# Performance work log

Hardware: AMD Instinct MI355X
Metric: run time of the kernel (lower is better)

Reference implementation:

```python
import jax, jax.numpy as jnp
import numpy as np

B, T, C, H, W = 4, 8, 128, 96, 96
D = 64  # d_model

def setup_inputs() -> dict:
    key = jax.random.key(0)
    ks = jax.random.split(key, 7)
    return {
        "x": jax.random.normal(ks[0], (B, T, C, H, W), dtype=jnp.float32),
        "Wq": jax.random.normal(ks[1], (D, C), dtype=jnp.float32) * (1.0 / np.sqrt(C)),
        "bq": jax.random.normal(ks[2], (D,), dtype=jnp.float32) * 0.01,
        "Wk": jax.random.normal(ks[3], (D, C), dtype=jnp.float32) * (1.0 / np.sqrt(C)),
        "bk": jax.random.normal(ks[4], (D,), dtype=jnp.float32) * 0.01,
        "Wv": jax.random.normal(ks[5], (C, C), dtype=jnp.float32) * (1.0 / np.sqrt(C)),
        "bv": jax.random.normal(ks[6], (C,), dtype=jnp.float32) * 0.01,
    }

def reference(x, Wq, bq, Wk, bk, Wv, bv):
    # x: (B, T, C, H, W). 1x1 convs == per-pixel channel matmuls.
    d_model = Wq.shape[0]
    scale = 1.0 / jnp.sqrt(jnp.asarray(d_model, x.dtype))
    # Project and land directly in (B, H, W, T, feat) layout (fuses the permutes).
    Q = jnp.einsum('btchw,dc->bhwtd', x, Wq) + bq  # (B,H,W,T,D)
    K = jnp.einsum('btchw,dc->bhwtd', x, Wk) + bk  # (B,H,W,T,D)
    V = jnp.einsum('btchw,ec->bhwte', x, Wv) + bv  # (B,H,W,T,C)
    scores = jnp.einsum('bhwtd,bhwsd->bhwts', Q, K) * scale  # (B,H,W,T,T)
    attn = jax.nn.softmax(scores, axis=-1)
    out = jnp.einsum('bhwts,bhwse->bhwte', attn, V)  # (B,H,W,T,C)
    return jnp.transpose(out, (0, 3, 4, 1, 2))  # (B,T,C,H,W)
```

## Files before the change

### kernel.cpp

```cpp
#include <hip/hip_runtime.h>
#include <hip/hip_bf16.h>

#define TT 8
#define CC 128
#define DD 64
#define HWp 9216
#define PP 16
#define NTILE 576
#define XB_STRIDE 152
#define QKV_STRIDE 264

typedef __attribute__((ext_vector_type(8))) short short8;
typedef __attribute__((ext_vector_type(4))) short short4v;
typedef __attribute__((ext_vector_type(4))) float floatx4;
typedef __attribute__((ext_vector_type(4))) unsigned uint4v;

__device__ __forceinline__ short f2bf(float f) {
    __hip_bfloat16 h = __float2bfloat16(f);
    return __builtin_bit_cast(short, h);
}
__device__ __forceinline__ float u2f(unsigned u) {
    return __builtin_bit_cast(float, u);
}
__device__ __forceinline__ void bf8_to_f(short8 v, float* f) {
    uint4v u = __builtin_bit_cast(uint4v, v);
#pragma unroll
    for (int i = 0; i < 4; ++i) {
        f[2 * i]     = u2f(u[i] << 16);
        f[2 * i + 1] = u2f(u[i] & 0xffff0000u);
    }
}

__global__ __launch_bounds__(512, 4) void ta_kernel(
    const float* __restrict__ x,
    const float* __restrict__ Wq, const float* __restrict__ bq,
    const float* __restrict__ Wk, const float* __restrict__ bk,
    const float* __restrict__ Wv, const float* __restrict__ bv,
    float* __restrict__ out)
{
    __shared__ short xb[32 * XB_STRIDE];
    __shared__ short qkv[TT * PP * QKV_STRIDE];

    const int tid  = threadIdx.x;
    const int wave = tid >> 6;
    const int lane = tid & 63;
    const int quad = lane >> 4;
    const int l16  = lane & 15;

    const int blk = blockIdx.x;
    const int b   = blk / NTILE;
    const int p0  = (blk % NTILE) * PP;

    short8 wfrag[2][4];
    float  bias[2][4];
#pragma unroll
    for (int i = 0; i < 2; ++i) {
        const int f0  = (wave * 2 + i) * 16;
        const int row = f0 + l16;
        const float* wrow;
        if (row < DD)            wrow = Wq + row * CC;
        else if (row < 2 * DD)   wrow = Wk + (row - DD) * CC;
        else                     wrow = Wv + (row - 2 * DD) * CC;
#pragma unroll
        for (int kc = 0; kc < 4; ++kc) {
            const float* src = wrow + kc * 32 + quad * 8;
            short8 v;
#pragma unroll
            for (int j = 0; j < 8; ++j) v[j] = f2bf(src[j]);
            wfrag[i][kc] = v;
        }
        const int fb = f0 + quad * 4;
        const float* bsrc; int off;
        if (fb < DD)            { bsrc = bq; off = fb; }
        else if (fb < 2 * DD)   { bsrc = bk; off = fb - DD; }
        else                    { bsrc = bv; off = fb - 2 * DD; }
#pragma unroll
        for (int r = 0; r < 4; ++r) bias[i][r] = bsrc[off + r];
    }

    const int c0 = tid >> 2;
    const int p4 = (tid & 3) * 4;
    const float* xsrc = x + ((size_t)(b * TT) * CC + c0) * HWp + p0 + p4;

    float4 cur0 = *(const float4*)xsrc;
    float4 cur1 = *(const float4*)(xsrc + (size_t)CC * HWp);
    for (int tp = 0; tp < 4; ++tp) {
        float4 nxt0 = cur0, nxt1 = cur1;
        if (tp < 3) {
            nxt0 = *(const float4*)(xsrc + (size_t)(2 * tp + 2) * CC * HWp);
            nxt1 = *(const float4*)(xsrc + (size_t)(2 * tp + 3) * CC * HWp);
        }

        __syncthreads();
        xb[(p4 + 0) * XB_STRIDE + c0] = f2bf(cur0.x);
        xb[(p4 + 1) * XB_STRIDE + c0] = f2bf(cur0.y);
        xb[(p4 + 2) * XB_STRIDE + c0] = f2bf(cur0.z);
        xb[(p4 + 3) * XB_STRIDE + c0] = f2bf(cur0.w);
        xb[(16 + p4 + 0) * XB_STRIDE + c0] = f2bf(cur1.x);
        xb[(16 + p4 + 1) * XB_STRIDE + c0] = f2bf(cur1.y);
        xb[(16 + p4 + 2) * XB_STRIDE + c0] = f2bf(cur1.z);
        xb[(16 + p4 + 3) * XB_STRIDE + c0] = f2bf(cur1.w);
        __syncthreads();

        floatx4 acc[2][2];
#pragma unroll
        for (int tt = 0; tt < 2; ++tt)
#pragma unroll
            for (int i = 0; i < 2; ++i)
#pragma unroll
                for (int r = 0; r < 4; ++r) acc[tt][i][r] = 0.f;
#pragma unroll
        for (int kc = 0; kc < 4; ++kc) {
            short8 xf0 = *(const short8*)&xb[l16 * XB_STRIDE + kc * 32 + quad * 8];
            short8 xf1 = *(const short8*)&xb[(16 + l16) * XB_STRIDE + kc * 32 + quad * 8];
            acc[0][0] = __builtin_amdgcn_mfma_f32_16x16x32_bf16(wfrag[0][kc], xf0, acc[0][0], 0, 0, 0);
            acc[0][1] = __builtin_amdgcn_mfma_f32_16x16x32_bf16(wfrag[1][kc], xf0, acc[0][1], 0, 0, 0);
            acc[1][0] = __builtin_amdgcn_mfma_f32_16x16x32_bf16(wfrag[0][kc], xf1, acc[1][0], 0, 0, 0);
            acc[1][1] = __builtin_amdgcn_mfma_f32_16x16x32_bf16(wfrag[1][kc], xf1, acc[1][1], 0, 0, 0);
        }
#pragma unroll
        for (int tt = 0; tt < 2; ++tt)
#pragma unroll
            for (int i = 0; i < 2; ++i) {
                const int f0 = (wave * 2 + i) * 16 + quad * 4;
                short4v o;
#pragma unroll
                for (int r = 0; r < 4; ++r) o[r] = f2bf(acc[tt][i][r] + bias[i][r]);
                *(short4v*)&qkv[((2 * tp + tt) * PP + l16) * QKV_STRIDE + f0] = o;
            }
        cur0 = nxt0; cur1 = nxt1;
    }
    __syncthreads();

    {
        const int p  = l16;
        const int tq = wave;

        const short* prow = &qkv[p * QKV_STRIDE];

        float qv[16];
        {
            const short* q8 = prow + (tq * PP) * QKV_STRIDE + quad * 16;
            bf8_to_f(*(const short8*)q8, qv);
            bf8_to_f(*(const short8*)(q8 + 8), qv + 8);
        }
        float sc[TT];
#pragma unroll
        for (int s = 0; s < TT; ++s) {
            const short* k8 = prow + (s * PP) * QKV_STRIDE + DD + quad * 16;
            float kv[16];
            bf8_to_f(*(const short8*)k8, kv);
            bf8_to_f(*(const short8*)(k8 + 8), kv + 8);
            float a = 0.f;
#pragma unroll
            for (int j = 0; j < 16; ++j) a = fmaf(qv[j], kv[j], a);
            sc[s] = a;
        }
#pragma unroll
        for (int m = 16; m <= 32; m <<= 1)
#pragma unroll
            for (int s = 0; s < TT; ++s) sc[s] += __shfl_xor(sc[s], m, 64);

        float mx = sc[0];
#pragma unroll
        for (int s = 1; s < TT; ++s) mx = fmaxf(mx, sc[s]);
        float sum = 0.f;
#pragma unroll
        for (int s = 0; s < TT; ++s) {
            float e = __expf((sc[s] - mx) * 0.125f);
            sc[s] = e; sum += e;
        }
        const float inv = 1.f / sum;
#pragma unroll
        for (int s = 0; s < TT; ++s) sc[s] *= inv;

        float o[32];
#pragma unroll
        for (int j = 0; j < 32; ++j) o[j] = 0.f;
#pragma unroll
        for (int s = 0; s < TT; ++s) {
            const short* vrow = prow + (s * PP) * QKV_STRIDE + 2 * DD + quad * 8;
            const float a = sc[s];
#pragma unroll
            for (int k = 0; k < 4; ++k) {
                float vv[8];
                bf8_to_f(*(const short8*)(vrow + k * 32), vv);
#pragma unroll
                for (int j = 0; j < 8; ++j) o[k * 8 + j] = fmaf(a, vv[j], o[k * 8 + j]);
            }
        }
        float* op = out + ((size_t)((b * TT + tq) * CC + quad * 8)) * HWp + p0 + p;
#pragma unroll
        for (int k = 0; k < 4; ++k)
#pragma unroll
            for (int j = 0; j < 8; ++j)
                op[(size_t)(k * 32 + j) * HWp] = o[k * 8 + j];
    }
}

extern "C" void kernel_launch(void* const* d_in, const int* in_sizes, int n_in,
                              void* d_out, int out_size, void* d_ws, size_t ws_size,
                              hipStream_t stream) {
    const float* x  = (const float*)d_in[0];
    const float* Wq = (const float*)d_in[1];
    const float* bq = (const float*)d_in[2];
    const float* Wk = (const float*)d_in[3];
    const float* bk = (const float*)d_in[4];
    const float* Wv = (const float*)d_in[5];
    const float* bv = (const float*)d_in[6];
    float* out = (float*)d_out;

    const int blocks = 4 * NTILE;
    ta_kernel<<<blocks, 512, 0, stream>>>(x, Wq, bq, Wk, bk, Wv, bv, out);
}
```

Before: 332.0 us.

## Process two pixel tiles per block with cross-tile prefetch and lighter barriers

Each block now covers two 16-pixel tiles, 32 pixels, in one 8-step loop, so the grid is half as large. The per-block conversion of the weight and bias fragments to bf16 is amortized over twice the work, and the next tile's x loads are prefetched across the tile boundary. `__syncthreads` is replaced by raw `s_barrier` calls wrapped in scheduling barriers, with an explicit lgkmcnt wait only where LDS writes must be visible. The K and V LDS reads in the attention phase are grouped to expose more memory-level parallelism. The trade-off is fewer blocks for latency hiding and more reliance on hand-placed barriers being correct.

```diff
diff --git a/kernel.cpp b/kernel.cpp
--- a/kernel.cpp
+++ b/kernel.cpp
@@ -6,7 +6,7 @@
 #define DD 64
 #define HWp 9216
 #define PP 16
-#define NTILE 576
+#define NBT 288
 #define XB_STRIDE 152
 #define QKV_STRIDE 264
 
@@ -29,6 +29,18 @@
         f[2 * i]     = u2f(u[i] << 16);
         f[2 * i + 1] = u2f(u[i] & 0xffff0000u);
     }
+}
+
+__device__ __forceinline__ void bar_raw() {
+    __builtin_amdgcn_sched_barrier(0);
+    __builtin_amdgcn_s_barrier();
+    __builtin_amdgcn_sched_barrier(0);
+}
+__device__ __forceinline__ void bar_lds() {
+    __builtin_amdgcn_sched_barrier(0);
+    asm volatile("s_waitcnt lgkmcnt(0)" ::: "memory");
+    __builtin_amdgcn_s_barrier();
+    __builtin_amdgcn_sched_barrier(0);
 }
 
 __global__ __launch_bounds__(512, 4) void ta_kernel(
@@ -48,8 +60,8 @@
     const int l16  = lane & 15;
 
     const int blk = blockIdx.x;
-    const int b   = blk / NTILE;
-    const int p0  = (blk % NTILE) * PP;
+    const int b   = blk / NBT;
+    const int p0b = (blk % NBT) * (2 * PP);
 
     short8 wfrag[2][4];
     float  bias[2][4];
@@ -80,18 +92,22 @@
 
     const int c0 = tid >> 2;
     const int p4 = (tid & 3) * 4;
-    const float* xsrc = x + ((size_t)(b * TT) * CC + c0) * HWp + p0 + p4;
+    const float* xsrc = x + ((size_t)(b * TT) * CC + c0) * HWp + p0b + p4;
 
     float4 cur0 = *(const float4*)xsrc;
     float4 cur1 = *(const float4*)(xsrc + (size_t)CC * HWp);
-    for (int tp = 0; tp < 4; ++tp) {
-        float4 nxt0 = cur0, nxt1 = cur1;
-        if (tp < 3) {
-            nxt0 = *(const float4*)(xsrc + (size_t)(2 * tp + 2) * CC * HWp);
-            nxt1 = *(const float4*)(xsrc + (size_t)(2 * tp + 3) * CC * HWp);
-        }
-
-        __syncthreads();
+    float4 nxt0 = cur0, nxt1 = cur1;
+
+    for (int r = 0; r < 8; ++r) {
+        const int tp = r & 3;
+        if (r < 7) {
+            const int nl = (r + 1) >> 2, np = (r + 1) & 3;
+            const float* ns = xsrc + nl * PP + (size_t)(2 * np) * CC * HWp;
+            nxt0 = *(const float4*)ns;
+            nxt1 = *(const float4*)(ns + (size_t)CC * HWp);
+        }
+
+        bar_raw();
         xb[(p4 + 0) * XB_STRIDE + c0] = f2bf(cur0.x);
         xb[(p4 + 1) * XB_STRIDE + c0] = f2bf(cur0.y);
         xb[(p4 + 2) * XB_STRIDE + c0] = f2bf(cur0.z);
@@ -100,7 +116,7 @@
         xb[(16 + p4 + 1) * XB_STRIDE + c0] = f2bf(cur1.y);
         xb[(16 + p4 + 2) * XB_STRIDE + c0] = f2bf(cur1.z);
         xb[(16 + p4 + 3) * XB_STRIDE + c0] = f2bf(cur1.w);
-        __syncthreads();
+        bar_lds();
 
         floatx4 acc[2][2];
 #pragma unroll
@@ -108,7 +124,7 @@
 #pragma unroll
             for (int i = 0; i < 2; ++i)
 #pragma unroll
-                for (int r = 0; r < 4; ++r) acc[tt][i][r] = 0.f;
+                for (int rr = 0; rr < 4; ++rr) acc[tt][i][rr] = 0.f;
 #pragma unroll
         for (int kc = 0; kc < 4; ++kc) {
             short8 xf0 = *(const short8*)&xb[l16 * XB_STRIDE + kc * 32 + quad * 8];
@@ -125,76 +141,96 @@
                 const int f0 = (wave * 2 + i) * 16 + quad * 4;
                 short4v o;
 #pragma unroll
-                for (int r = 0; r < 4; ++r) o[r] = f2bf(acc[tt][i][r] + bias[i][r]);
+                for (int rr = 0; rr < 4; ++rr) o[rr] = f2bf(acc[tt][i][rr] + bias[i][rr]);
                 *(short4v*)&qkv[((2 * tp + tt) * PP + l16) * QKV_STRIDE + f0] = o;
             }
         cur0 = nxt0; cur1 = nxt1;
-    }
-    __syncthreads();
-
-    {
-        const int p  = l16;
-        const int tq = wave;
-
-        const short* prow = &qkv[p * QKV_STRIDE];
-
-        float qv[16];
-        {
-            const short* q8 = prow + (tq * PP) * QKV_STRIDE + quad * 16;
-            bf8_to_f(*(const short8*)q8, qv);
-            bf8_to_f(*(const short8*)(q8 + 8), qv + 8);
-        }
-        float sc[TT];
-#pragma unroll
-        for (int s = 0; s < TT; ++s) {
-            const short* k8 = prow + (s * PP) * QKV_STRIDE + DD + quad * 16;
-            float kv[16];
-            bf8_to_f(*(const short8*)k8, kv);
-            bf8_to_f(*(const short8*)(k8 + 8), kv + 8);
-            float a = 0.f;
-#pragma unroll
-            for (int j = 0; j < 16; ++j) a = fmaf(qv[j], kv[j], a);
-            sc[s] = a;
-        }
-#pragma unroll
-        for (int m = 16; m <= 32; m <<= 1)
-#pragma unroll
-            for (int s = 0; s < TT; ++s) sc[s] += __shfl_xor(sc[s], m, 64);
-
-        float mx = sc[0];
-#pragma unroll
-        for (int s = 1; s < TT; ++s) mx = fmaxf(mx, sc[s]);
-        float sum = 0.f;
-#pragma unroll
-        for (int s = 0; s < TT; ++s) {
-            float e = __expf((sc[s] - mx) * 0.125f);
-            sc[s] = e; sum += e;
-        }
-        const float inv = 1.f / sum;
-#pragma unroll
-        for (int s = 0; s < TT; ++s) sc[s] *= inv;
-
-        float o[32];
-#pragma unroll
-        for (int j = 0; j < 32; ++j) o[j] = 0.f;
-#pragma unroll
-        for (int s = 0; s < TT; ++s) {
-            const short* vrow = prow + (s * PP) * QKV_STRIDE + 2 * DD + quad * 8;
-            const float a = sc[s];
-#pragma unroll
-            for (int k = 0; k < 4; ++k) {
+
+        if (tp == 3) {
+            bar_lds();
+
+            const int p0t = p0b + (r >> 2) * PP;
+            const int p   = l16;
+            const int tq  = wave;
+            const short* prow = &qkv[p * QKV_STRIDE];
+
+            float qv[16];
+            {
+                const short* q8 = prow + (tq * PP) * QKV_STRIDE + quad * 16;
+                bf8_to_f(*(const short8*)q8, qv);
+                bf8_to_f(*(const short8*)(q8 + 8), qv + 8);
+            }
+            float sc[TT];
+#pragma unroll
+            for (int h = 0; h < 2; ++h) {
+                short8 kr[8];
+#pragma unroll
+                for (int s4 = 0; s4 < 4; ++s4) {
+                    const short* k8 = prow + ((h * 4 + s4) * PP) * QKV_STRIDE + DD + quad * 16;
+                    kr[2 * s4]     = *(const short8*)k8;
+                    kr[2 * s4 + 1] = *(const short8*)(k8 + 8);
+                }
+#pragma unroll
+                for (int s4 = 0; s4 < 4; ++s4) {
+                    float kv[16];
+                    bf8_to_f(kr[2 * s4], kv);
+                    bf8_to_f(kr[2 * s4 + 1], kv + 8);
+                    float a = 0.f;
+#pragma unroll
+                    for (int j = 0; j < 16; ++j) a = fmaf(qv[j], kv[j], a);
+                    sc[h * 4 + s4] = a;
+                }
+            }
+#pragma unroll
+            for (int m = 16; m <= 32; m <<= 1)
+#pragma unroll
+                for (int s = 0; s < TT; ++s) sc[s] += __shfl_xor(sc[s], m, 64);
+
+            float mx = sc[0];
+#pragma unroll
+            for (int s = 1; s < TT; ++s) mx = fmaxf(mx, sc[s]);
+            float sum = 0.f;
+#pragma unroll
+            for (int s = 0; s < TT; ++s) {
+                float e = __expf((sc[s] - mx) * 0.125f);
+                sc[s] = e; sum += e;
+            }
+            const float inv = 1.f / sum;
+#pragma unroll
+            for (int s = 0; s < TT; ++s) sc[s] *= inv;
+
+            float o[32];
+#pragma unroll
+            for (int j = 0; j < 32; ++j) o[j] = 0.f;
+#pragma unroll
+            for (int s = 0; s < TT; ++s) {
+                const short* vrow = prow + (s * PP) * QKV_STRIDE + 2 * DD + quad * 8;
+                short8 v0 = *(const short8*)(vrow);
+                short8 v1 = *(const short8*)(vrow + 32);
+                short8 v2 = *(const short8*)(vrow + 64);
+                short8 v3 = *(const short8*)(vrow + 96);
+                const float a = sc[s];
                 float vv[8];
-                bf8_to_f(*(const short8*)(vrow + k * 32), vv);
-#pragma unroll
-                for (int j = 0; j < 8; ++j) o[k * 8 + j] = fmaf(a, vv[j], o[k * 8 + j]);
-            }
-        }
-        float* op = out + ((size_t)((b * TT + tq) * CC + quad * 8)) * HWp + p0 + p;
-#pragma unroll
-        for (int k = 0; k < 4; ++k)
-#pragma unroll
-            for (int j = 0; j < 8; ++j)
-                op[(size_t)(k * 32 + j) * HWp] = o[k * 8 + j];
+                bf8_to_f(v0, vv);
+#pragma unroll
+                for (int j = 0; j < 8; ++j) o[j] = fmaf(a, vv[j], o[j]);
+                bf8_to_f(v1, vv);
+#pragma unroll
+                for (int j = 0; j < 8; ++j) o[8 + j] = fmaf(a, vv[j], o[8 + j]);
+                bf8_to_f(v2, vv);
+#pragma unroll
+                for (int j = 0; j < 8; ++j) o[16 + j] = fmaf(a, vv[j], o[16 + j]);
+                bf8_to_f(v3, vv);
+#pragma unroll
+                for (int j = 0; j < 8; ++j) o[24 + j] = fmaf(a, vv[j], o[24 + j]);
+            }
+            float* op = out + ((size_t)((b * TT + tq) * CC + quad * 8)) * HWp + p0t + p;
+#pragma unroll
+            for (int k = 0; k < 4; ++k)
+#pragma unroll
+                for (int j = 0; j < 8; ++j)
+                    op[(size_t)(k * 32 + j) * HWp] = o[k * 8 + j];
+        }
     }
 }
 
@@ -210,6 +246,6 @@
     const float* bv = (const float*)d_in[6];
     float* out = (float*)d_out;
 
-    const int blocks = 4 * NTILE;
+    const int blocks = 4 * NBT;
     ta_kernel<<<blocks, 512, 0, stream>>>(x, Wq, bq, Wk, bk, Wv, bv, out);
 }
```

Measured after the change: 352.2 us. +6.1%, slower.
